# Optimization experiments

Measured on AMD Instinct MI355X. Metric: run time of the kernel, lower is better.

Reference implementation:

```python
import jax, jax.numpy as jnp
import numpy as np

B, S, D = 32, 1024, 1024   # batch, seq_len, d_model
P, F = 4, 4096             # num_phases, d_ff
# Each phase owns a contiguous split of S/P sequence positions (set_splits builds
# a disjoint contiguous partition of the sequence; assert t == seq_length).


def setup_inputs() -> dict:
    key = jax.random.key(0)
    ks = jax.random.split(key, 6)
    x = jax.random.normal(ks[0], (B, S, D), dtype=jnp.float32)
    phases = jax.random.randint(ks[1], (B, S), 0, P, dtype=jnp.int32)
    s1 = 1.0 / np.sqrt(D)
    s2 = 1.0 / np.sqrt(F)
    W1 = jax.random.uniform(ks[2], (P, D, F), jnp.float32, -s1, s1)
    b1 = jax.random.uniform(ks[3], (P, F), jnp.float32, -s1, s1)
    W2 = jax.random.uniform(ks[4], (P, F, D), jnp.float32, -s2, s2)
    b2 = jax.random.uniform(ks[5], (P, D), jnp.float32, -s2, s2)
    return {"x": x, "W1": W1, "b1": b1, "W2": W2, "b2": b2, "phases": phases}


def reference(x, W1, b1, W2, b2, phases):
    # Branched path (phases.ndim > 1): gather each phase's contiguous split,
    # run that phase's FF, scatter back. Since the static phase_mask is a
    # contiguous equal partition, gather/scatter == reshape into [B, P, S/P, D].
    xs = x.reshape(B, P, S // P, D)
    h = jax.nn.relu(jnp.einsum('bpsd,pdf->bpsf', xs, W1) + b1[None, :, None, :])
    y = jnp.einsum('bpsf,pfd->bpsd', h, W2) + b2[None, :, None, :]
    return y.reshape(B, S, D)
```

## Files before the change

kernel.cpp:

```cpp
#include <hip/hip_runtime.h>
#include <hip/hip_bf16.h>
#include <stdint.h>

typedef __bf16 bf16_t;
typedef bf16_t bf16x8 __attribute__((ext_vector_type(8)));
typedef bf16_t bf16x4 __attribute__((ext_vector_type(4)));
typedef float  f32x4  __attribute__((ext_vector_type(4)));

#define AS1(p) ((const __attribute__((address_space(1))) void*)(p))
#define AS3(p) ((__attribute__((address_space(3))) void*)(p))

static constexpr int B_ = 32, S_ = 1024, D_ = 1024, P_ = 4, F_ = 4096;
static constexpr int SPP = S_ / P_;
static constexpr int MP  = B_ * SPP;

__global__ void conv_x_kernel(const float* __restrict__ x, bf16_t* __restrict__ xg) {
  const int64_t n4 = (int64_t)B_ * S_ * D_ / 4;
  for (int64_t i = (int64_t)blockIdx.x * blockDim.x + threadIdx.x; i < n4;
       i += (int64_t)gridDim.x * blockDim.x) {
    int64_t e = i << 2;
    int d = (int)(e & (D_ - 1));
    int s = (int)((e >> 10) & (S_ - 1));
    int b = (int)(e >> 20);
    int p = s >> 8;
    int r = (b << 8) | (s & 255);
    const float4 v = ((const float4*)x)[i];
    bf16x4 o;
    o[0] = (bf16_t)v.x; o[1] = (bf16_t)v.y; o[2] = (bf16_t)v.z; o[3] = (bf16_t)v.w;
    *(bf16x4*)&xg[(((int64_t)p * MP + r) << 10) | d] = o;
  }
}

__global__ void conv_wt_kernel(const float* __restrict__ W, bf16_t* __restrict__ Wt,
                               int K, int N) {
  __shared__ bf16_t tile[32][33];
  const int p = blockIdx.z;
  const float* Wp = W + (int64_t)p * K * N;
  bf16_t* Wtp = Wt + (int64_t)p * K * N;
  const int n0 = blockIdx.x * 32, k0 = blockIdx.y * 32;
  const int tx = threadIdx.x & 31, ty = threadIdx.x >> 5;
  #pragma unroll
  for (int j = 0; j < 4; ++j) {
    int kr = ty + j * 8;
    tile[kr][tx] = (bf16_t)Wp[(int64_t)(k0 + kr) * N + n0 + tx];
  }
  __syncthreads();
  #pragma unroll
  for (int j = 0; j < 4; ++j) {
    int nr = ty + j * 8;
    Wtp[(int64_t)(n0 + nr) * K + k0 + tx] = tile[tx][nr];
  }
}


__device__ __forceinline__ bf16x8 ldsfrag(const char* region, int row, int cb) {
  return *(const bf16x8*)(region + row * 128 + (cb ^ ((row & 7) << 4)));
}

template<int LDK>
__device__ __forceinline__ void stage_half(const bf16_t* gsrc, char* ldsreg, int t) {
  #pragma unroll
  for (int j = 0; j < 2; ++j) {
    const int idx = j * 512 + t;
    const int row = idx >> 3;
    const int cb  = ((idx & 7) << 4) ^ ((row & 7) << 4);
    __builtin_amdgcn_global_load_lds(AS1((const char*)(gsrc + (int64_t)row * LDK) + cb),
                                     AS3(ldsreg + idx * 16), 16, 0, 0);
  }
}

#define MFMA_QUAD(AF, BF, MO, NO) \
  do { _Pragma("unroll") for (int k_ = 0; k_ < 2; ++k_) \
       _Pragma("unroll") for (int m_ = 0; m_ < 4; ++m_) \
       _Pragma("unroll") for (int n_ = 0; n_ < 2; ++n_) \
         acc[(MO) + m_][(NO) + n_] = __builtin_amdgcn_mfma_f32_16x16x32_bf16( \
             AF[m_][k_], BF[n_][k_], acc[(MO) + m_][(NO) + n_], 0, 0, 0); } while (0)

#define FRAG_A(DST, BUF, MO) \
  do { _Pragma("unroll") for (int m_ = 0; m_ < 4; ++m_) { \
         DST[m_][0] = *(const bf16x8*)(baseA_k0 + (BUF) * 32768 + ((MO) + m_) * 2048); \
         DST[m_][1] = *(const bf16x8*)(baseA_k1 + (BUF) * 32768 + ((MO) + m_) * 2048); } } while (0)

#define FRAG_B(DST, BUF, NO) \
  do { _Pragma("unroll") for (int n_ = 0; n_ < 2; ++n_) { \
         DST[n_][0] = *(const bf16x8*)(baseB_k0 + (BUF) * 32768 + ((NO) + n_) * 2048); \
         DST[n_][1] = *(const bf16x8*)(baseB_k1 + (BUF) * 32768 + ((NO) + n_) * 2048); } } while (0)

#define BAR()   __builtin_amdgcn_s_barrier()
#define SBAR()  __builtin_amdgcn_sched_barrier(0)
#define PRIO(x) __builtin_amdgcn_s_setprio(x)
#define VMCNT0() asm volatile("s_waitcnt vmcnt(0)" ::: "memory")

template<bool RELU, bool OUT_BF16, int KK, int NN>
__global__ __launch_bounds__(512, 2)
void ffgemm8_kernel(const bf16_t* __restrict__ A, const bf16_t* __restrict__ Bt,
                    const float* __restrict__ bias, void* __restrict__ outv, int M) {
  static_assert(KK % 128 == 0, "need even number of 64-wide K tiles");
  __shared__ __align__(16) char smem[131072];
  char* const At0 = smem;
  char* const At1 = smem + 32768;
  char* const Bs0 = smem + 65536;
  char* const Bs1 = smem + 98304;

  const int t = threadIdx.x, lane = t & 63, w = t >> 6;
  const int wm = w >> 2, wn = w & 3;
  const int fr = lane & 15, hi = lane >> 4;

  const int xorm = (fr & 7) << 4;
  const char* const baseA_k0 = At0 + (wm * 128 + fr) * 128 + ((hi * 16) ^ xorm);
  const char* const baseA_k1 = At0 + (wm * 128 + fr) * 128 + ((64 + hi * 16) ^ xorm);
  const char* const baseB_k0 = Bs0 + (wn * 64 + fr) * 128 + ((hi * 16) ^ xorm);
  const char* const baseB_k1 = Bs0 + (wn * 64 + fr) * 128 + ((64 + hi * 16) ^ xorm);

  const int gx = gridDim.x, gy = gridDim.y;
  const int nwg = gx * gy * (int)gridDim.z;
  const int id  = ((int)blockIdx.z * gy + (int)blockIdx.y) * gx + (int)blockIdx.x;
  const int swz = (id & 7) * (nwg >> 3) + (id >> 3);
  const int per_p = gx * gy;
  const int p  = swz / per_p;
  const int q  = swz % per_p;
  const int band = q / (gx * 4), qq = q % (gx * 4);
  const int bx = qq >> 2, by = band * 4 + (qq & 3);

  const int tile_m = by * 256, tile_n = bx * 256;
  const bf16_t* Ab = A  + (int64_t)p * M  * KK + (int64_t)tile_m * KK;
  const bf16_t* Bb = Bt + (int64_t)p * NN * KK + (int64_t)tile_n * KK;
  const float* biasp = bias + (int64_t)p * NN;

  f32x4 acc[8][4] = {};
  constexpr int NI2 = KK / 128;

  stage_half<KK>(Ab,                       At0,          t);
  stage_half<KK>(Ab + (int64_t)128 * KK,   At0 + 16384,  t);
  stage_half<KK>(Bb,                       Bs0,          t);
  stage_half<KK>(Bb + (int64_t)128 * KK,   Bs0 + 16384,  t);
  VMCNT0();
  BAR(); SBAR();

  for (int j = 0; j < NI2; ++j) {
    const int kX = j * 128;
    const bool more = (j < NI2 - 1);
    bf16x8 a0[4][2], a1[4][2], b0[2][2], b1[2][2];

    FRAG_A(a0, 0, 0); FRAG_B(b0, 0, 0); FRAG_B(b1, 0, 2);
    stage_half<KK>(Ab + (kX + 64),                      At1,          t);
    stage_half<KK>(Ab + (int64_t)128 * KK + (kX + 64),  At1 + 16384,  t);
    stage_half<KK>(Bb + (kX + 64),                      Bs1,          t);
    stage_half<KK>(Bb + (int64_t)128 * KK + (kX + 64),  Bs1 + 16384,  t);
    PRIO(1); MFMA_QUAD(a0, b0, 0, 0); PRIO(0); SBAR();
    FRAG_A(a1, 0, 4);
    PRIO(1); MFMA_QUAD(a0, b1, 0, 2); PRIO(0); SBAR();
    PRIO(1); MFMA_QUAD(a1, b0, 4, 0); PRIO(0); SBAR();
    PRIO(1); MFMA_QUAD(a1, b1, 4, 2); PRIO(0);
    VMCNT0();
    SBAR(); BAR();

    FRAG_A(a0, 1, 0); FRAG_B(b0, 1, 0); FRAG_B(b1, 1, 2);
    if (more) {
      stage_half<KK>(Ab + (kX + 128),                     At0,          t);
      stage_half<KK>(Ab + (int64_t)128 * KK + (kX + 128), At0 + 16384,  t);
      stage_half<KK>(Bb + (kX + 128),                     Bs0,          t);
      stage_half<KK>(Bb + (int64_t)128 * KK + (kX + 128), Bs0 + 16384,  t);
    }
    PRIO(1); MFMA_QUAD(a0, b0, 0, 0); PRIO(0); SBAR();
    FRAG_A(a1, 1, 4);
    PRIO(1); MFMA_QUAD(a0, b1, 0, 2); PRIO(0); SBAR();
    PRIO(1); MFMA_QUAD(a1, b0, 4, 0); PRIO(0); SBAR();
    PRIO(1); MFMA_QUAD(a1, b1, 4, 2); PRIO(0);
    if (more) VMCNT0();
    SBAR(); BAR();
  }

  float bv[4];
  #pragma unroll
  for (int n = 0; n < 4; ++n) bv[n] = biasp[tile_n + wn * 64 + n * 16 + fr];
  if (OUT_BF16) {
    bf16_t* out = (bf16_t*)outv + (int64_t)p * M * NN;
    #pragma unroll
    for (int m = 0; m < 8; ++m)
      #pragma unroll
      for (int j2 = 0; j2 < 4; ++j2) {
        const int row = tile_m + wm * 128 + m * 16 + hi * 4 + j2;
        #pragma unroll
        for (int n = 0; n < 4; ++n) {
          const int col = tile_n + wn * 64 + n * 16 + fr;
          float v = acc[m][n][j2] + bv[n];
          if (RELU) v = fmaxf(v, 0.0f);
          out[(int64_t)row * NN + col] = (bf16_t)v;
        }
      }
  } else {
    float* out = (float*)outv;
    #pragma unroll
    for (int m = 0; m < 8; ++m)
      #pragma unroll
      for (int j2 = 0; j2 < 4; ++j2) {
        const int row = tile_m + wm * 128 + m * 16 + hi * 4 + j2;
        const int grow = ((row >> 8) << 10) + p * SPP + (row & 255);
        #pragma unroll
        for (int n = 0; n < 4; ++n) {
          const int col = tile_n + wn * 64 + n * 16 + fr;
          out[(int64_t)grow * NN + col] = acc[m][n][j2] + bv[n];
        }
      }
  }
}

extern "C" void kernel_launch(void* const* d_in, const int* in_sizes, int n_in,
                              void* d_out, int out_size, void* d_ws, size_t ws_size,
                              hipStream_t stream) {
  (void)in_sizes; (void)n_in; (void)out_size; (void)ws_size;
  const float* x  = (const float*)d_in[0];
  const float* W1 = (const float*)d_in[1];
  const float* b1 = (const float*)d_in[2];
  const float* W2 = (const float*)d_in[3];
  const float* b2 = (const float*)d_in[4];
  float* y = (float*)d_out;

  char* ws = (char*)d_ws;
  bf16_t* xg = (bf16_t*)ws;
  bf16_t* wt = (bf16_t*)(ws + (size_t)64 * 1024 * 1024);
  bf16_t* h  = (bf16_t*)(ws + (size_t)96 * 1024 * 1024);

  conv_x_kernel<<<2048, 256, 0, stream>>>(x, xg);
  conv_wt_kernel<<<dim3(F_ / 32, D_ / 32, P_), 256, 0, stream>>>(W1, wt, D_, F_);
  ffgemm8_kernel<true, true, 1024, 4096><<<dim3(F_ / 256, MP / 256, P_), 512, 0, stream>>>(
      xg, wt, b1, h, MP);
  conv_wt_kernel<<<dim3(D_ / 32, F_ / 32, P_), 256, 0, stream>>>(W2, wt, F_, D_);
  ffgemm8_kernel<false, false, 4096, 1024><<<dim3(D_ / 256, MP / 256, P_), 512, 0, stream>>>(
      h, wt, b2, y, MP);
}
```

Before: 610.6 us.

## Load B fragments directly from global into registers, halve LDS usage

The B operand is no longer staged through LDS. Each thread loads its bf16x8 B fragments straight from global memory into registers and prefetches the next K tile during the MFMAs, while only A stays double-buffered in LDS (64KB instead of 128KB). The loop now runs one 64-wide K tile per iteration, uses a partial vmcnt wait, and reorders MFMAs so the B registers can be refilled early. This removes the LDS write/read traffic for B and could allow more occupancy, but the direct global loads are uncoalesced per-lane 16-byte reads with long latency that may stall the MFMAs.

```diff
diff --git a/kernel.cpp b/kernel.cpp
--- a/kernel.cpp
+++ b/kernel.cpp
@@ -70,9 +70,9 @@
 }
 
 #define MFMA_QUAD(AF, BF, MO, NO) \
-  do { _Pragma("unroll") for (int k_ = 0; k_ < 2; ++k_) \
-       _Pragma("unroll") for (int m_ = 0; m_ < 4; ++m_) \
+  do { _Pragma("unroll") for (int m_ = 0; m_ < 4; ++m_) \
        _Pragma("unroll") for (int n_ = 0; n_ < 2; ++n_) \
+       _Pragma("unroll") for (int k_ = 0; k_ < 2; ++k_) \
          acc[(MO) + m_][(NO) + n_] = __builtin_amdgcn_mfma_f32_16x16x32_bf16( \
              AF[m_][k_], BF[n_][k_], acc[(MO) + m_][(NO) + n_], 0, 0, 0); } while (0)
 
@@ -81,14 +81,15 @@
          DST[m_][0] = *(const bf16x8*)(baseA_k0 + (BUF) * 32768 + ((MO) + m_) * 2048); \
          DST[m_][1] = *(const bf16x8*)(baseA_k1 + (BUF) * 32768 + ((MO) + m_) * 2048); } } while (0)
 
-#define FRAG_B(DST, BUF, NO) \
-  do { _Pragma("unroll") for (int n_ = 0; n_ < 2; ++n_) { \
-         DST[n_][0] = *(const bf16x8*)(baseB_k0 + (BUF) * 32768 + ((NO) + n_) * 2048); \
-         DST[n_][1] = *(const bf16x8*)(baseB_k1 + (BUF) * 32768 + ((NO) + n_) * 2048); } } while (0)
+#define LOAD_B(DST, K0, NO) \
+  do { _Pragma("unroll") for (int n_ = 0; n_ < 2; ++n_) \
+       _Pragma("unroll") for (int ks_ = 0; ks_ < 2; ++ks_) \
+         DST[n_][ks_] = *(const bf16x8*)(Bt_th + ((NO) + n_) * 16 * KK + (K0) + ks_ * 32); } while (0)
 
 #define BAR()   __builtin_amdgcn_s_barrier()
 #define SBAR()  __builtin_amdgcn_sched_barrier(0)
 #define PRIO(x) __builtin_amdgcn_s_setprio(x)
+#define VMCNT8() asm volatile("s_waitcnt vmcnt(8)" ::: "memory")
 #define VMCNT0() asm volatile("s_waitcnt vmcnt(0)" ::: "memory")
 
 template<bool RELU, bool OUT_BF16, int KK, int NN>
@@ -96,11 +97,8 @@
 void ffgemm8_kernel(const bf16_t* __restrict__ A, const bf16_t* __restrict__ Bt,
                     const float* __restrict__ bias, void* __restrict__ outv, int M) {
   static_assert(KK % 128 == 0, "need even number of 64-wide K tiles");
-  __shared__ __align__(16) char smem[131072];
+  __shared__ __align__(16) char smem[65536];
   char* const At0 = smem;
-  char* const At1 = smem + 32768;
-  char* const Bs0 = smem + 65536;
-  char* const Bs1 = smem + 98304;
 
   const int t = threadIdx.x, lane = t & 63, w = t >> 6;
   const int wm = w >> 2, wn = w & 3;
@@ -109,8 +107,6 @@
   const int xorm = (fr & 7) << 4;
   const char* const baseA_k0 = At0 + (wm * 128 + fr) * 128 + ((hi * 16) ^ xorm);
   const char* const baseA_k1 = At0 + (wm * 128 + fr) * 128 + ((64 + hi * 16) ^ xorm);
-  const char* const baseB_k0 = Bs0 + (wn * 64 + fr) * 128 + ((hi * 16) ^ xorm);
-  const char* const baseB_k1 = Bs0 + (wn * 64 + fr) * 128 + ((64 + hi * 16) ^ xorm);
 
   const int gx = gridDim.x, gy = gridDim.y;
   const int nwg = gx * gy * (int)gridDim.z;
@@ -126,48 +122,39 @@
   const bf16_t* Ab = A  + (int64_t)p * M  * KK + (int64_t)tile_m * KK;
   const bf16_t* Bb = Bt + (int64_t)p * NN * KK + (int64_t)tile_n * KK;
   const float* biasp = bias + (int64_t)p * NN;
+  const bf16_t* const Bt_th = Bb + (int64_t)(wn * 64 + fr) * KK + hi * 8;
 
   f32x4 acc[8][4] = {};
-  constexpr int NI2 = KK / 128;
+  constexpr int NT = KK / 64;
+
+  bf16x8 a0[4][2], a1[4][2], b0[2][2], b1[2][2];
 
   stage_half<KK>(Ab,                       At0,          t);
   stage_half<KK>(Ab + (int64_t)128 * KK,   At0 + 16384,  t);
-  stage_half<KK>(Bb,                       Bs0,          t);
-  stage_half<KK>(Bb + (int64_t)128 * KK,   Bs0 + 16384,  t);
+  LOAD_B(b0, 0, 0);
+  LOAD_B(b1, 0, 2);
   VMCNT0();
   BAR(); SBAR();
 
-  for (int j = 0; j < NI2; ++j) {
-    const int kX = j * 128;
-    const bool more = (j < NI2 - 1);
-    bf16x8 a0[4][2], a1[4][2], b0[2][2], b1[2][2];
-
-    FRAG_A(a0, 0, 0); FRAG_B(b0, 0, 0); FRAG_B(b1, 0, 2);
-    stage_half<KK>(Ab + (kX + 64),                      At1,          t);
-    stage_half<KK>(Ab + (int64_t)128 * KK + (kX + 64),  At1 + 16384,  t);
-    stage_half<KK>(Bb + (kX + 64),                      Bs1,          t);
-    stage_half<KK>(Bb + (int64_t)128 * KK + (kX + 64),  Bs1 + 16384,  t);
+  #pragma unroll 2
+  for (int ti = 0; ti < NT; ++ti) {
+    const int c   = ti & 1;
+    const int kn  = (ti + 1) * 64;
+    const bool nxt = (ti + 1 < NT);
+
+    if (nxt) { stage_half<KK>(Ab + kn,                     At0 + (c ^ 1) * 32768,         t);
+               stage_half<KK>(Ab + (int64_t)128 * KK + kn, At0 + (c ^ 1) * 32768 + 16384, t); }
+    SBAR();
+    FRAG_A(a0, c, 0);
     PRIO(1); MFMA_QUAD(a0, b0, 0, 0); PRIO(0); SBAR();
-    FRAG_A(a1, 0, 4);
+    FRAG_A(a1, c, 4);
+    PRIO(1); MFMA_QUAD(a1, b0, 4, 0); PRIO(0); SBAR();
+    if (nxt) LOAD_B(b0, kn, 0);
+    SBAR();
     PRIO(1); MFMA_QUAD(a0, b1, 0, 2); PRIO(0); SBAR();
-    PRIO(1); MFMA_QUAD(a1, b0, 4, 0); PRIO(0); SBAR();
     PRIO(1); MFMA_QUAD(a1, b1, 4, 2); PRIO(0);
-    VMCNT0();
-    SBAR(); BAR();
-
-    FRAG_A(a0, 1, 0); FRAG_B(b0, 1, 0); FRAG_B(b1, 1, 2);
-    if (more) {
-      stage_half<KK>(Ab + (kX + 128),                     At0,          t);
-      stage_half<KK>(Ab + (int64_t)128 * KK + (kX + 128), At0 + 16384,  t);
-      stage_half<KK>(Bb + (kX + 128),                     Bs0,          t);
-      stage_half<KK>(Bb + (int64_t)128 * KK + (kX + 128), Bs0 + 16384,  t);
-    }
-    PRIO(1); MFMA_QUAD(a0, b0, 0, 0); PRIO(0); SBAR();
-    FRAG_A(a1, 1, 4);
-    PRIO(1); MFMA_QUAD(a0, b1, 0, 2); PRIO(0); SBAR();
-    PRIO(1); MFMA_QUAD(a1, b0, 4, 0); PRIO(0); SBAR();
-    PRIO(1); MFMA_QUAD(a1, b1, 4, 2); PRIO(0);
-    if (more) VMCNT0();
+    if (nxt) LOAD_B(b1, kn, 2);
+    if (nxt) VMCNT8(); else VMCNT0();
     SBAR(); BAR();
   }
 
```

Result: slower. 777.2 us (+27.3%).
